# Kernel tuning notes

Measured on AMD Instinct MI355X. Metric: run time of the kernel, lower is better.

The kernel has to match this reference:

```python
import jax, jax.numpy as jnp
import numpy as np

NUM_HEADS = 12


def setup_inputs() -> dict:
    key = jax.random.key(0)
    ks = jax.random.split(key, 6)
    C = 768
    hd = C // NUM_HEADS  # 64
    H = W = 32
    x = jax.random.normal(ks[0], (4, H, W, C), dtype=jnp.float32)
    # Linear weights stored as (in, out) so y = x @ W (+ b)
    Wqkv = jax.random.normal(ks[1], (C, 3 * C), dtype=jnp.float32) * 0.02
    Wproj = jax.random.normal(ks[2], (C, C), dtype=jnp.float32) * 0.02
    bproj = jax.random.normal(ks[3], (C,), dtype=jnp.float32) * 0.02
    rel_pos_h = jax.random.normal(ks[4], (2 * H - 1, hd), dtype=jnp.float32) * 0.02
    rel_pos_w = jax.random.normal(ks[5], (2 * W - 1, hd), dtype=jnp.float32) * 0.02
    return {"x": x, "Wqkv": Wqkv, "Wproj": Wproj, "bproj": bproj,
            "rel_pos_h": rel_pos_h, "rel_pos_w": rel_pos_w}


def _get_rel_pos(size: int, rel_pos: jnp.ndarray) -> jnp.ndarray:
    # q_size == k_size == size; table already has 2*size-1 entries -> no interpolation
    coords = jnp.arange(size)[:, None] - jnp.arange(size)[None, :] + (size - 1)
    return rel_pos[coords]  # (size, size, head_dim)


def reference(x, Wqkv, Wproj, bproj, rel_pos_h, rel_pos_w):
    B, H, W, C = x.shape
    hn = NUM_HEADS
    hd = C // hn
    scale = hd ** (-0.5)
    S = H * W

    qkv = x @ Wqkv                                   # (B,H,W,3C)
    qkv = qkv.reshape(B, S, 3, hn, hd)
    qkv = jnp.transpose(qkv, (2, 0, 3, 1, 4)).reshape(3, B * hn, S, hd)
    q, k, v = qkv[0], qkv[1], qkv[2]                 # each (B*hn, S, hd)

    # decomposed relative position bias
    Rh = _get_rel_pos(H, rel_pos_h)                  # (H,H,hd)
    Rw = _get_rel_pos(W, rel_pos_w)                  # (W,W,hd)
    r_q = q.reshape(B * hn, H, W, hd)
    rel_h = jnp.einsum('bhwc,hkc->bhwk', r_q, Rh)    # (B*hn,H,W,H)
    rel_w = jnp.einsum('bhwc,wkc->bhwk', r_q, Rw)    # (B*hn,H,W,W)
    bias = rel_h[..., :, None] + rel_w[..., None, :] # (B*hn,H,W,H,W)
    bias = bias.reshape(B * hn, S, S)

    scores = scale * jnp.einsum('bqc,bkc->bqk', q, k) + bias
    attn = jax.nn.softmax(scores, axis=-1)
    out = jnp.einsum('bqk,bkc->bqc', attn, v)        # (B*hn,S,hd)

    out = out.reshape(B, hn, H, W, hd)
    out = jnp.transpose(out, (0, 2, 3, 1, 4)).reshape(B, H, W, C)
    return out @ Wproj + bproj
```

## Files before the change

kernel.cpp:

```cpp
#include <hip/hip_runtime.h>
#include <stddef.h>

typedef __bf16 bf16x8 __attribute__((ext_vector_type(8)));
typedef __bf16 bf16x4 __attribute__((ext_vector_type(4)));
typedef float  f32x4  __attribute__((ext_vector_type(4)));

#define MFMA16(a, b, c) __builtin_amdgcn_mfma_f32_16x16x32_bf16((a), (b), (c), 0, 0, 0)

__device__ __forceinline__ void gload_lds16(const void* gsrc, void* ldst) {
    __builtin_amdgcn_global_load_lds(
        (__attribute__((address_space(1))) void*)gsrc,
        (__attribute__((address_space(3))) void*)ldst,
        16, 0, 0);
}

__global__ void prep_kernel(const float* __restrict__ x, __bf16* __restrict__ xbf,
                            const float* __restrict__ Wqkv, __bf16* __restrict__ WqkvT,
                            const float* __restrict__ Wproj, __bf16* __restrict__ WprojT) {
    __shared__ float tile[32][33];
    const int bx = blockIdx.x, tid = threadIdx.x;
    if (bx < 3072) {
        int i = bx * 256 + tid;
        float4 v = ((const float4*)x)[i];
        bf16x4 o = {(__bf16)v.x, (__bf16)v.y, (__bf16)v.z, (__bf16)v.w};
        ((bf16x4*)xbf)[i] = o;
        return;
    }
    const float* in; __bf16* out; int R, C, c0, r0;
    if (bx < 4800) { int bb = bx - 3072; in = Wqkv;  out = WqkvT;  R = 768; C = 2304;
                     c0 = (bb % 72) * 32; r0 = (bb / 72) * 32; }
    else           { int bb = bx - 4800; in = Wproj; out = WprojT; R = 768; C = 768;
                     c0 = (bb % 24) * 32; r0 = (bb / 24) * 32; }
    const int tx = tid & 31, ty = tid >> 5;
#pragma unroll
    for (int i = 0; i < 32; i += 8)
        tile[ty + i][tx] = in[(size_t)(r0 + ty + i) * C + c0 + tx];
    __syncthreads();
#pragma unroll
    for (int i = 0; i < 32; i += 8)
        out[(size_t)(c0 + ty + i) * R + r0 + tx] = (__bf16)tile[tx][ty + i];
}

__device__ __forceinline__ void gemm_core_bk64(
    const __bf16* __restrict__ A, const __bf16* __restrict__ Bt, int K,
    int m0, int n0, __bf16* aT, __bf16* bT, f32x4 acc[4][4]) {
    const int tid  = threadIdx.x;
    const int wid  = tid >> 6, lane = tid & 63;
    const int quad = lane >> 4, l16 = lane & 15;
    const int wm = (wid >> 1) * 64, wn = (wid & 1) * 64;
    const int r_in = lane >> 3;
    const int cswz = ((lane & 7) ^ r_in) * 8;
    const __bf16* gA = A  + (size_t)(m0 + wid * 8 + r_in) * K + cswz;
    const __bf16* gB = Bt + (size_t)(n0 + wid * 8 + r_in) * K + cswz;
    const int sA = (l16 & 7);
    for (int k0 = 0; k0 < K; k0 += 64) {
        __syncthreads();
#pragma unroll
        for (int j = 0; j < 4; j++) {
            gload_lds16(gA + (size_t)(j * 32) * K + k0, aT + (j * 32 + wid * 8) * 64);
            gload_lds16(gB + (size_t)(j * 32) * K + k0, bT + (j * 32 + wid * 8) * 64);
        }
        __syncthreads();
#pragma unroll
        for (int kh = 0; kh < 2; kh++) {
            bf16x8 af[4], bfr[4];
#pragma unroll
            for (int t = 0; t < 4; t++) {
                const int slot = ((kh * 4 + quad) ^ sA) << 3;
                af[t]  = *(const bf16x8*)(aT + (wm + t * 16 + l16) * 64 + slot);
                bfr[t] = *(const bf16x8*)(bT + (wn + t * 16 + l16) * 64 + slot);
            }
#pragma unroll
            for (int rt = 0; rt < 4; rt++)
#pragma unroll
                for (int ct = 0; ct < 4; ct++)
                    acc[rt][ct] = MFMA16(af[rt], bfr[ct], acc[rt][ct]);
        }
    }
}

__global__ __launch_bounds__(256, 3)
void gemm_qkv_kernel(const __bf16* __restrict__ A, const __bf16* __restrict__ Bt,
                     __bf16* __restrict__ qb, __bf16* __restrict__ kb,
                     __bf16* __restrict__ vtb) {
    __shared__ __bf16 aT[8192], bT[8192];
    f32x4 acc[4][4];
#pragma unroll
    for (int i = 0; i < 4; i++)
#pragma unroll
        for (int j = 0; j < 4; j++) { f32x4 z = {0.f, 0.f, 0.f, 0.f}; acc[i][j] = z; }
    const int m0 = blockIdx.x * 128, n0 = blockIdx.y * 128;
    gemm_core_bk64(A, Bt, 768, m0, n0, aT, bT, acc);
    const int tid = threadIdx.x, wid = tid >> 6, lane = tid & 63;
    const int quad = lane >> 4, l16 = lane & 15;
    const int wm = (wid >> 1) * 64, wn = (wid & 1) * 64;
#pragma unroll
    for (int rt = 0; rt < 4; rt++)
#pragma unroll
        for (int ct = 0; ct < 4; ct++) {
            const int ng = n0 + wn + ct * 16 + l16;
            const int which = ng / 768;
            const int rem = ng - which * 768;
            const int hh = rem >> 6, d = rem & 63;
#pragma unroll
            for (int r = 0; r < 4; r++) {
                const int mg = m0 + wm + rt * 16 + quad * 4 + r;
                const int b = mg >> 10, s = mg & 1023;
                const int bh = b * 12 + hh;
                __bf16 bv = (__bf16)acc[rt][ct][r];
                if (which == 0)      qb[((size_t)bh * 1024 + s) * 64 + d] = bv;
                else if (which == 1) kb[((size_t)bh * 1024 + s) * 64 + d] = bv;
                else                 vtb[((size_t)bh * 64 + d) * 1024 + s] = bv;
            }
        }
}

__global__ __launch_bounds__(256, 3)
void gemm_proj_kernel(const __bf16* __restrict__ A, const __bf16* __restrict__ Bt,
                      const float* __restrict__ bias, float* __restrict__ out) {
    __shared__ __bf16 aT[8192], bT[8192];
    f32x4 acc[4][4];
#pragma unroll
    for (int i = 0; i < 4; i++)
#pragma unroll
        for (int j = 0; j < 4; j++) { f32x4 z = {0.f, 0.f, 0.f, 0.f}; acc[i][j] = z; }
    const int m0 = blockIdx.x * 128, n0 = blockIdx.y * 128;
    gemm_core_bk64(A, Bt, 768, m0, n0, aT, bT, acc);
    const int tid = threadIdx.x, wid = tid >> 6, lane = tid & 63;
    const int quad = lane >> 4, l16 = lane & 15;
    const int wm = (wid >> 1) * 64, wn = (wid & 1) * 64;
#pragma unroll
    for (int rt = 0; rt < 4; rt++)
#pragma unroll
        for (int ct = 0; ct < 4; ct++) {
            const int ng = n0 + wn + ct * 16 + l16;
            const float bb = bias[ng];
#pragma unroll
            for (int r = 0; r < 4; r++) {
                const int mg = m0 + wm + rt * 16 + quad * 4 + r;
                out[(size_t)mg * 768 + ng] = acc[rt][ct][r] + bb;
            }
        }
}

__global__ __launch_bounds__(256, 2)
void relpos_kernel(const __bf16* __restrict__ q, const float* __restrict__ rph,
                   const float* __restrict__ rpw, float* __restrict__ rel_h,
                   float* __restrict__ rel_w) {
    const int tid = threadIdx.x, wid = tid >> 6, lane = tid & 63;
    const int quad = lane >> 4, l16 = lane & 15;
    const int bx = blockIdx.x;
    const int isW = blockIdx.y;
    const int bh = bx >> 5, fix = bx & 31;
    const int mi = (wid >> 1) * 16, ni = (wid & 1) * 16;
    const int m = mi + l16;
    const int s_a = isW ? (m * 32 + fix) : (fix * 32 + m);
    const __bf16* qp = q + ((size_t)bh * 1024 + s_a) * 64;
    bf16x8 a0 = *(const bf16x8*)(qp + quad * 8);
    bf16x8 a1 = *(const bf16x8*)(qp + 32 + quad * 8);
    const int n = ni + l16;
    const float* tb = (isW ? rpw : rph) + (size_t)(fix - n + 31) * 64;
    float4 t0 = *(const float4*)(tb + quad * 8);
    float4 t1 = *(const float4*)(tb + quad * 8 + 4);
    float4 t2 = *(const float4*)(tb + 32 + quad * 8);
    float4 t3 = *(const float4*)(tb + 32 + quad * 8 + 4);
    bf16x8 b0 = {(__bf16)t0.x, (__bf16)t0.y, (__bf16)t0.z, (__bf16)t0.w,
                 (__bf16)t1.x, (__bf16)t1.y, (__bf16)t1.z, (__bf16)t1.w};
    bf16x8 b1 = {(__bf16)t2.x, (__bf16)t2.y, (__bf16)t2.z, (__bf16)t2.w,
                 (__bf16)t3.x, (__bf16)t3.y, (__bf16)t3.z, (__bf16)t3.w};
    f32x4 acc = {0.f, 0.f, 0.f, 0.f};
    acc = MFMA16(a0, b0, acc);
    acc = MFMA16(a1, b1, acc);
    float* op = isW ? rel_w : rel_h;
#pragma unroll
    for (int r = 0; r < 4; r++) {
        int mo = mi + quad * 4 + r;
        int so = isW ? (mo * 32 + fix) : (fix * 32 + mo);
        op[((size_t)bh * 1024 + so) * 32 + n] = acc[r];
    }
}

__global__ __launch_bounds__(256, 3)
void attn_kernel(const __bf16* __restrict__ q, const __bf16* __restrict__ kk,
                 const __bf16* __restrict__ vt, const float* __restrict__ rel_h,
                 const float* __restrict__ rel_w, __bf16* __restrict__ aout) {
    __shared__ __bf16 kbuf[4096];
    __shared__ __bf16 vbuf[4096];
    __shared__ __bf16 pbuf[4][32 * 72];
    __shared__ float  relh[128][32];
    const int tid = threadIdx.x, wid = tid >> 6, lane = tid & 63;
    const int quad = lane >> 4, l16 = lane & 15;
    const int qt = blockIdx.x, bh = blockIdx.y;
    const int b = bh / 12, hh = bh - b * 12;
    const int q0 = qt * 128;
    const int w0 = wid * 32;

    {
        int rr = tid >> 1, cc = (tid & 1) * 16;
        const float* sh = rel_h + ((size_t)bh * 1024 + q0 + rr) * 32 + cc;
        *(float4*)(&relh[rr][cc])      = *(const float4*)sh;
        *(float4*)(&relh[rr][cc + 4])  = *(const float4*)(sh + 4);
        *(float4*)(&relh[rr][cc + 8])  = *(const float4*)(sh + 8);
        *(float4*)(&relh[rr][cc + 12]) = *(const float4*)(sh + 12);
    }

    float bw[2][2][4];
#pragma unroll
    for (int rt = 0; rt < 2; rt++)
#pragma unroll
        for (int r = 0; r < 4; r++) {
            const float* pw = rel_w + ((size_t)bh * 1024 + q0 + w0 + rt * 16 + quad * 4 + r) * 32;
            bw[rt][0][r] = pw[l16];
            bw[rt][1][r] = pw[16 + l16];
        }

    bf16x8 aq[2][2];
#pragma unroll
    for (int rt = 0; rt < 2; rt++) {
        const __bf16* qp = q + ((size_t)bh * 1024 + q0 + w0 + rt * 16 + l16) * 64;
        aq[rt][0] = *(const bf16x8*)(qp + quad * 8);
        aq[rt][1] = *(const bf16x8*)(qp + 32 + quad * 8);
    }

    float l_run[2][4];
    f32x4 o_acc[2][4];
#pragma unroll
    for (int rt = 0; rt < 2; rt++)
#pragma unroll
        for (int r = 0; r < 4; r++) l_run[rt][r] = 0.f;
#pragma unroll
    for (int rt = 0; rt < 2; rt++)
#pragma unroll
        for (int t = 0; t < 4; t++) { f32x4 z = {0.f, 0.f, 0.f, 0.f}; o_acc[rt][t] = z; }

    const __bf16* kg0 = kk + (size_t)bh * 65536;
    const __bf16* vg0 = vt + (size_t)bh * 65536;
    const int c1 = wid, c2 = wid + 4;
    const int srow = lane >> 3;
    const int scol = ((lane & 7) ^ srow) * 8;
    const int swz0 = ((quad ^ (l16 & 7)) << 3);
    const int swz1 = (((quad | 4) ^ (l16 & 7)) << 3);
    __bf16* pw = pbuf[wid];

    __syncthreads();

    for (int kt = 0; kt < 16; kt++) {
        __syncthreads();
        const __bf16* kg = kg0 + kt * 64 * 64;
        const __bf16* vg = vg0 + kt * 64;
        gload_lds16(kg + (c1 * 8 + srow) * 64 + scol, kbuf + c1 * 512);
        gload_lds16(kg + (c2 * 8 + srow) * 64 + scol, kbuf + c2 * 512);
        gload_lds16(vg + (size_t)(c1 * 8 + srow) * 1024 + scol, vbuf + c1 * 512);
        gload_lds16(vg + (size_t)(c2 * 8 + srow) * 1024 + scol, vbuf + c2 * 512);
        __syncthreads();

        bf16x8 bk[4][2];
#pragma unroll
        for (int ct = 0; ct < 4; ct++) {
            const int key = ct * 16 + l16;
            bk[ct][0] = *(const bf16x8*)(kbuf + key * 64 + swz0);
            bk[ct][1] = *(const bf16x8*)(kbuf + key * 64 + swz1);
        }

#pragma unroll
        for (int rt = 0; rt < 2; rt++) {
            f32x4 sacc[4];
#pragma unroll
            for (int ct = 0; ct < 4; ct++) {
                f32x4 z = {0.f, 0.f, 0.f, 0.f};
                z = MFMA16(aq[rt][0], bk[ct][0], z);
                z = MFMA16(aq[rt][1], bk[ct][1], z);
                sacc[ct] = z;
            }
            float bh0[4], bh1[4];
#pragma unroll
            for (int r = 0; r < 4; r++) {
                bh0[r] = relh[w0 + rt * 16 + quad * 4 + r][kt * 2];
                bh1[r] = relh[w0 + rt * 16 + quad * 4 + r][kt * 2 + 1];
            }
#pragma unroll
            for (int ct = 0; ct < 4; ct++)
#pragma unroll
                for (int r = 0; r < 4; r++) {
                    float sv = fmaf(sacc[ct][r], 0.125f,
                                    (ct < 2 ? bh0[r] : bh1[r]) +
                                    ((ct & 1) ? bw[rt][1][r] : bw[rt][0][r]));
                    float p = __expf(sv);
                    l_run[rt][r] += p;
                    pw[(rt * 16 + quad * 4 + r) * 72 + ct * 16 + l16] = (__bf16)p;
                }
        }

#pragma unroll
        for (int nt = 0; nt < 4; nt++) {
            const int d = nt * 16 + l16;
            bf16x8 bv0 = *(const bf16x8*)(vbuf + d * 64 + swz0);
            bf16x8 bv1 = *(const bf16x8*)(vbuf + d * 64 + swz1);
#pragma unroll
            for (int rt = 0; rt < 2; rt++) {
                bf16x8 ap0 = *(const bf16x8*)(pw + (rt * 16 + l16) * 72 + quad * 8);
                bf16x8 ap1 = *(const bf16x8*)(pw + (rt * 16 + l16) * 72 + 32 + quad * 8);
                o_acc[rt][nt] = MFMA16(ap0, bv0, o_acc[rt][nt]);
                o_acc[rt][nt] = MFMA16(ap1, bv1, o_acc[rt][nt]);
            }
        }
    }

#pragma unroll
    for (int rt = 0; rt < 2; rt++)
#pragma unroll
        for (int r = 0; r < 4; r++) {
            float s = l_run[rt][r];
            s += __shfl_xor(s, 1);
            s += __shfl_xor(s, 2);
            s += __shfl_xor(s, 4);
            s += __shfl_xor(s, 8);
            l_run[rt][r] = 1.f / s;
        }
#pragma unroll
    for (int rt = 0; rt < 2; rt++) {
        const int srow_o = q0 + w0 + rt * 16 + quad * 4;
#pragma unroll
        for (int nt = 0; nt < 4; nt++)
#pragma unroll
            for (int r = 0; r < 4; r++) {
                float v = o_acc[rt][nt][r] * l_run[rt][r];
                aout[((size_t)b * 1024 + srow_o + r) * 768 + hh * 64 + nt * 16 + l16] = (__bf16)v;
            }
    }
}

extern "C" void kernel_launch(void* const* d_in, const int* in_sizes, int n_in,
                              void* d_out, int out_size, void* d_ws, size_t ws_size,
                              hipStream_t stream) {
    const float* x     = (const float*)d_in[0];
    const float* Wqkv  = (const float*)d_in[1];
    const float* Wproj = (const float*)d_in[2];
    const float* bproj = (const float*)d_in[3];
    const float* rph   = (const float*)d_in[4];
    const float* rpw   = (const float*)d_in[5];
    float* out = (float*)d_out;
    char* ws = (char*)d_ws;

    __bf16* xbf    = (__bf16*)(ws);
    __bf16* WqkvT  = (__bf16*)(ws + 6291456);
    __bf16* WprojT = (__bf16*)(ws + 9830400);
    __bf16* qb     = (__bf16*)(ws + 11010048);
    __bf16* kb     = (__bf16*)(ws + 17301504);
    __bf16* vtb    = (__bf16*)(ws + 23592960);
    float*  rel_h  = (float*)(ws + 29884416);
    float*  rel_w  = (float*)(ws + 36175872);
    __bf16* aob    = (__bf16*)(ws + 42467328);

    prep_kernel<<<dim3(5376), dim3(256), 0, stream>>>(x, xbf, Wqkv, WqkvT, Wproj, WprojT);
    gemm_qkv_kernel<<<dim3(32, 18), dim3(256), 0, stream>>>(xbf, WqkvT, qb, kb, vtb);
    relpos_kernel<<<dim3(1536, 2), dim3(256), 0, stream>>>(qb, rph, rpw, rel_h, rel_w);
    attn_kernel<<<dim3(8, 48), dim3(256), 0, stream>>>(qb, kb, vtb, rel_h, rel_w, aob);
    gemm_proj_kernel<<<dim3(32, 6), dim3(256), 0, stream>>>(aob, WprojT, bproj, out);
}
```

Before: 165.8 us.

## Fuse relative-position bias into attention kernel and double-buffer K/V loads

Drops the separate relpos kernel and computes the rel_h and rel_w projections inside the attention kernel with MFMA, using the rel_pos tables directly. rel_w is found by multiplying q against all 63 table rows and then reading out the diagonal band. This removes one kernel launch and the global round trip of the rel_h/rel_w buffers. It also double-buffers the K/V LDS tiles so the next tile's loads are issued before the current tile is computed, dropping one barrier per iteration. In exchange, LDS use rises, which may cut occupancy; launch bounds change from 3 to 2 blocks per CU.

```diff
diff --git a/kernel.cpp b/kernel.cpp
--- a/kernel.cpp
+++ b/kernel.cpp
@@ -144,75 +144,19 @@
 }
 
 __global__ __launch_bounds__(256, 2)
-void relpos_kernel(const __bf16* __restrict__ q, const float* __restrict__ rph,
-                   const float* __restrict__ rpw, float* __restrict__ rel_h,
-                   float* __restrict__ rel_w) {
-    const int tid = threadIdx.x, wid = tid >> 6, lane = tid & 63;
-    const int quad = lane >> 4, l16 = lane & 15;
-    const int bx = blockIdx.x;
-    const int isW = blockIdx.y;
-    const int bh = bx >> 5, fix = bx & 31;
-    const int mi = (wid >> 1) * 16, ni = (wid & 1) * 16;
-    const int m = mi + l16;
-    const int s_a = isW ? (m * 32 + fix) : (fix * 32 + m);
-    const __bf16* qp = q + ((size_t)bh * 1024 + s_a) * 64;
-    bf16x8 a0 = *(const bf16x8*)(qp + quad * 8);
-    bf16x8 a1 = *(const bf16x8*)(qp + 32 + quad * 8);
-    const int n = ni + l16;
-    const float* tb = (isW ? rpw : rph) + (size_t)(fix - n + 31) * 64;
-    float4 t0 = *(const float4*)(tb + quad * 8);
-    float4 t1 = *(const float4*)(tb + quad * 8 + 4);
-    float4 t2 = *(const float4*)(tb + 32 + quad * 8);
-    float4 t3 = *(const float4*)(tb + 32 + quad * 8 + 4);
-    bf16x8 b0 = {(__bf16)t0.x, (__bf16)t0.y, (__bf16)t0.z, (__bf16)t0.w,
-                 (__bf16)t1.x, (__bf16)t1.y, (__bf16)t1.z, (__bf16)t1.w};
-    bf16x8 b1 = {(__bf16)t2.x, (__bf16)t2.y, (__bf16)t2.z, (__bf16)t2.w,
-                 (__bf16)t3.x, (__bf16)t3.y, (__bf16)t3.z, (__bf16)t3.w};
-    f32x4 acc = {0.f, 0.f, 0.f, 0.f};
-    acc = MFMA16(a0, b0, acc);
-    acc = MFMA16(a1, b1, acc);
-    float* op = isW ? rel_w : rel_h;
-#pragma unroll
-    for (int r = 0; r < 4; r++) {
-        int mo = mi + quad * 4 + r;
-        int so = isW ? (mo * 32 + fix) : (fix * 32 + mo);
-        op[((size_t)bh * 1024 + so) * 32 + n] = acc[r];
-    }
-}
-
-__global__ __launch_bounds__(256, 3)
 void attn_kernel(const __bf16* __restrict__ q, const __bf16* __restrict__ kk,
-                 const __bf16* __restrict__ vt, const float* __restrict__ rel_h,
-                 const float* __restrict__ rel_w, __bf16* __restrict__ aout) {
-    __shared__ __bf16 kbuf[4096];
-    __shared__ __bf16 vbuf[4096];
+                 const __bf16* __restrict__ vt, const float* __restrict__ rph,
+                 const float* __restrict__ rpw, __bf16* __restrict__ aout) {
+    __shared__ __bf16 kv[2][8192];
     __shared__ __bf16 pbuf[4][32 * 72];
-    __shared__ float  relh[128][32];
+    __shared__ float  relh[128][33];
     const int tid = threadIdx.x, wid = tid >> 6, lane = tid & 63;
     const int quad = lane >> 4, l16 = lane & 15;
     const int qt = blockIdx.x, bh = blockIdx.y;
     const int b = bh / 12, hh = bh - b * 12;
     const int q0 = qt * 128;
     const int w0 = wid * 32;
-
-    {
-        int rr = tid >> 1, cc = (tid & 1) * 16;
-        const float* sh = rel_h + ((size_t)bh * 1024 + q0 + rr) * 32 + cc;
-        *(float4*)(&relh[rr][cc])      = *(const float4*)sh;
-        *(float4*)(&relh[rr][cc + 4])  = *(const float4*)(sh + 4);
-        *(float4*)(&relh[rr][cc + 8])  = *(const float4*)(sh + 8);
-        *(float4*)(&relh[rr][cc + 12]) = *(const float4*)(sh + 12);
-    }
-
-    float bw[2][2][4];
-#pragma unroll
-    for (int rt = 0; rt < 2; rt++)
-#pragma unroll
-        for (int r = 0; r < 4; r++) {
-            const float* pw = rel_w + ((size_t)bh * 1024 + q0 + w0 + rt * 16 + quad * 4 + r) * 32;
-            bw[rt][0][r] = pw[l16];
-            bw[rt][1][r] = pw[16 + l16];
-        }
+    const int h = qt * 4 + wid;
 
     bf16x8 aq[2][2];
 #pragma unroll
@@ -221,6 +165,63 @@
         aq[rt][0] = *(const bf16x8*)(qp + quad * 8);
         aq[rt][1] = *(const bf16x8*)(qp + 32 + quad * 8);
     }
+
+    float* Dw = ((float*)kv) + wid * 2048;
+#pragma unroll
+    for (int ct = 0; ct < 4; ct++) {
+        int j = ct * 16 + l16; if (j > 62) j = 62;
+        const float* tb = rpw + (size_t)j * 64;
+        float4 t0 = *(const float4*)(tb + quad * 8);
+        float4 t1 = *(const float4*)(tb + quad * 8 + 4);
+        float4 t2 = *(const float4*)(tb + 32 + quad * 8);
+        float4 t3 = *(const float4*)(tb + 32 + quad * 8 + 4);
+        bf16x8 b0 = {(__bf16)t0.x, (__bf16)t0.y, (__bf16)t0.z, (__bf16)t0.w,
+                     (__bf16)t1.x, (__bf16)t1.y, (__bf16)t1.z, (__bf16)t1.w};
+        bf16x8 b1 = {(__bf16)t2.x, (__bf16)t2.y, (__bf16)t2.z, (__bf16)t2.w,
+                     (__bf16)t3.x, (__bf16)t3.y, (__bf16)t3.z, (__bf16)t3.w};
+#pragma unroll
+        for (int rt = 0; rt < 2; rt++) {
+            f32x4 z = {0.f, 0.f, 0.f, 0.f};
+            z = MFMA16(aq[rt][0], b0, z);
+            z = MFMA16(aq[rt][1], b1, z);
+#pragma unroll
+            for (int i = 0; i < 4; i++)
+                Dw[(rt * 16 + quad * 4 + i) * 64 + ct * 16 + l16] = z[i];
+        }
+    }
+#pragma unroll
+    for (int ct = 0; ct < 2; ct++) {
+        const int tr = h - (ct * 16 + l16) + 31;
+        const float* tb = rph + (size_t)tr * 64;
+        float4 t0 = *(const float4*)(tb + quad * 8);
+        float4 t1 = *(const float4*)(tb + quad * 8 + 4);
+        float4 t2 = *(const float4*)(tb + 32 + quad * 8);
+        float4 t3 = *(const float4*)(tb + 32 + quad * 8 + 4);
+        bf16x8 b0 = {(__bf16)t0.x, (__bf16)t0.y, (__bf16)t0.z, (__bf16)t0.w,
+                     (__bf16)t1.x, (__bf16)t1.y, (__bf16)t1.z, (__bf16)t1.w};
+        bf16x8 b1 = {(__bf16)t2.x, (__bf16)t2.y, (__bf16)t2.z, (__bf16)t2.w,
+                     (__bf16)t3.x, (__bf16)t3.y, (__bf16)t3.z, (__bf16)t3.w};
+#pragma unroll
+        for (int rt = 0; rt < 2; rt++) {
+            f32x4 z = {0.f, 0.f, 0.f, 0.f};
+            z = MFMA16(aq[rt][0], b0, z);
+            z = MFMA16(aq[rt][1], b1, z);
+#pragma unroll
+            for (int i = 0; i < 4; i++)
+                relh[w0 + rt * 16 + quad * 4 + i][ct * 16 + l16] = z[i];
+        }
+    }
+    __syncthreads();
+    float bw[2][2][4];
+#pragma unroll
+    for (int rt = 0; rt < 2; rt++)
+#pragma unroll
+        for (int r = 0; r < 4; r++) {
+            const int row = rt * 16 + quad * 4 + r;
+            bw[rt][0][r] = Dw[row * 64 + row - l16 + 31];
+            bw[rt][1][r] = Dw[row * 64 + row + 15 - l16];
+        }
+    __syncthreads();
 
     float l_run[2][4];
     f32x4 o_acc[2][4];
@@ -242,17 +243,24 @@
     const int swz1 = (((quad | 4) ^ (l16 & 7)) << 3);
     __bf16* pw = pbuf[wid];
 
-    __syncthreads();
-
+    auto stage = [&](int buf, int kt) {
+        const __bf16* kg = kg0 + kt * 4096;
+        const __bf16* vg = vg0 + kt * 64;
+        __bf16* kb_ = &kv[buf][0];
+        __bf16* vb_ = &kv[buf][4096];
+        gload_lds16(kg + (c1 * 8 + srow) * 64 + scol, kb_ + c1 * 512);
+        gload_lds16(kg + (c2 * 8 + srow) * 64 + scol, kb_ + c2 * 512);
+        gload_lds16(vg + (size_t)(c1 * 8 + srow) * 1024 + scol, vb_ + c1 * 512);
+        gload_lds16(vg + (size_t)(c2 * 8 + srow) * 1024 + scol, vb_ + c2 * 512);
+    };
+
+    stage(0, 0);
     for (int kt = 0; kt < 16; kt++) {
+        const int cur = kt & 1;
         __syncthreads();
-        const __bf16* kg = kg0 + kt * 64 * 64;
-        const __bf16* vg = vg0 + kt * 64;
-        gload_lds16(kg + (c1 * 8 + srow) * 64 + scol, kbuf + c1 * 512);
-        gload_lds16(kg + (c2 * 8 + srow) * 64 + scol, kbuf + c2 * 512);
-        gload_lds16(vg + (size_t)(c1 * 8 + srow) * 1024 + scol, vbuf + c1 * 512);
-        gload_lds16(vg + (size_t)(c2 * 8 + srow) * 1024 + scol, vbuf + c2 * 512);
-        __syncthreads();
+        if (kt < 15) stage(1 - cur, kt + 1);
+        const __bf16* kbuf = &kv[cur][0];
+        const __bf16* vbuf = &kv[cur][4096];
 
         bf16x8 bk[4][2];
 #pragma unroll
@@ -348,13 +356,10 @@
     __bf16* qb     = (__bf16*)(ws + 11010048);
     __bf16* kb     = (__bf16*)(ws + 17301504);
     __bf16* vtb    = (__bf16*)(ws + 23592960);
-    float*  rel_h  = (float*)(ws + 29884416);
-    float*  rel_w  = (float*)(ws + 36175872);
-    __bf16* aob    = (__bf16*)(ws + 42467328);
+    __bf16* aob    = (__bf16*)(ws + 29884416);
 
     prep_kernel<<<dim3(5376), dim3(256), 0, stream>>>(x, xbf, Wqkv, WqkvT, Wproj, WprojT);
     gemm_qkv_kernel<<<dim3(32, 18), dim3(256), 0, stream>>>(xbf, WqkvT, qb, kb, vtb);
-    relpos_kernel<<<dim3(1536, 2), dim3(256), 0, stream>>>(qb, rph, rpw, rel_h, rel_w);
-    attn_kernel<<<dim3(8, 48), dim3(256), 0, stream>>>(qb, kb, vtb, rel_h, rel_w, aob);
+    attn_kernel<<<dim3(8, 48), dim3(256), 0, stream>>>(qb, kb, vtb, rph, rpw, aob);
     gemm_proj_kernel<<<dim3(32, 6), dim3(256), 0, stream>>>(aob, WprojT, bproj, out);
 }
```

Measured after the change: 161.7 us. 2.5% less time.
